# Kernel tuning notes

Measured on AMD Instinct MI355X. Metric: run time of the kernel, lower is better.

Reference implementation:

```python
import jax, jax.numpy as jnp
import numpy as np

N_EMBD = 1024
N_HEAD = 16
HEAD_DIM = N_EMBD // N_HEAD
B, T = 2, 2048
EPS = 1e-5


def setup_inputs() -> dict:
    key = jax.random.key(0)
    ks = jax.random.split(key, 12)
    s = lambda fan_in: 1.0 / np.sqrt(fan_in)
    return {
        "x": jax.random.normal(ks[0], (B, T, N_EMBD), dtype=jnp.float32),
        "ln1_g": jnp.ones((N_EMBD,), jnp.float32),
        "ln1_b": jnp.zeros((N_EMBD,), jnp.float32),
        "W_attn": jax.random.normal(ks[1], (N_EMBD, 3 * N_EMBD), jnp.float32) * s(N_EMBD),
        "b_attn": jnp.zeros((3 * N_EMBD,), jnp.float32),
        "W_proj": jax.random.normal(ks[2], (N_EMBD, N_EMBD), jnp.float32) * s(N_EMBD),
        "b_proj": jnp.zeros((N_EMBD,), jnp.float32),
        "ln2_g": jnp.ones((N_EMBD,), jnp.float32),
        "ln2_b": jnp.zeros((N_EMBD,), jnp.float32),
        "W_fc": jax.random.normal(ks[3], (N_EMBD, 4 * N_EMBD), jnp.float32) * s(N_EMBD),
        "b_fc": jnp.zeros((4 * N_EMBD,), jnp.float32),
        "W_fc2": jax.random.normal(ks[4], (4 * N_EMBD, N_EMBD), jnp.float32) * s(4 * N_EMBD),
        "b_fc2": jnp.zeros((N_EMBD,), jnp.float32),
    }


def _layernorm(x, g, b):
    mu = jnp.mean(x, axis=-1, keepdims=True)
    var = jnp.mean(jnp.square(x - mu), axis=-1, keepdims=True)
    return (x - mu) * jax.lax.rsqrt(var + EPS) * g + b


def _attention(x, W_attn, b_attn, W_proj, b_proj):
    Bsz, Tlen, C = x.shape
    qkv = x @ W_attn + b_attn  # [B,T,3C]
    q, k, v = jnp.split(qkv, 3, axis=-1)
    # [B,H,T,D]
    q = q.reshape(Bsz, Tlen, N_HEAD, HEAD_DIM).transpose(0, 2, 1, 3)
    k = k.reshape(Bsz, Tlen, N_HEAD, HEAD_DIM).transpose(0, 2, 1, 3)
    v = v.reshape(Bsz, Tlen, N_HEAD, HEAD_DIM).transpose(0, 2, 1, 3)
    att = jnp.einsum("bhqd,bhkd->bhqk", q, k) * (HEAD_DIM ** -0.5)
    causal = jnp.tril(jnp.ones((Tlen, Tlen), dtype=bool))
    att = jnp.where(causal[None, None], att, -jnp.inf)
    att = jax.nn.softmax(att, axis=-1)
    y = jnp.einsum("bhqk,bhkd->bhqd", att, v)
    y = y.transpose(0, 2, 1, 3).reshape(Bsz, Tlen, C)
    return y @ W_proj + b_proj


def _mlp(x, W_fc, b_fc, W_fc2, b_fc2):
    h = jax.nn.gelu(x @ W_fc + b_fc, approximate=False)
    return h @ W_fc2 + b_fc2


def reference(x, ln1_g, ln1_b, W_attn, b_attn, W_proj, b_proj,
              ln2_g, ln2_b, W_fc, b_fc, W_fc2, b_fc2):
    x = x + _attention(_layernorm(x, ln1_g, ln1_b), W_attn, b_attn, W_proj, b_proj)
    x = x + _mlp(_layernorm(x, ln2_g, ln2_b), W_fc, b_fc, W_fc2, b_fc2)
    return x
```

## Files before the change

kernel.cpp:

```cpp
#include <hip/hip_runtime.h>
#include <math.h>

typedef unsigned short ushort_t;
typedef __attribute__((ext_vector_type(8))) short f16x8;
typedef __attribute__((ext_vector_type(4))) float f32x4;

#define N_EMBD 1024
#define N_HEAD 16
#define HEAD_DIM 64
#define SEQ_B 2
#define SEQ_T 2048
#define M_TOK (SEQ_B * SEQ_T)

__device__ __forceinline__ ushort_t f2b(float f) {
    union { float f; unsigned int u; } v; v.f = f;
    unsigned int r = (v.u + 0x7FFFu + ((v.u >> 16) & 1u)) >> 16;
    return (ushort_t)r;
}

__device__ __forceinline__ float gelu_fast(float v) {
    float u = v + 0.044715f * v * v * v;
    float e = __expf(-1.5957691216057308f * u);
    return v * __frcp_rn(1.0f + e);
}

__device__ __forceinline__ void gload_lds16(const ushort_t* g, ushort_t* l) {
    __builtin_amdgcn_global_load_lds(
        (const __attribute__((address_space(1))) void*)g,
        (__attribute__((address_space(3))) void*)l, 16, 0, 0);
}

__global__ __launch_bounds__(256) void prep_w(
    const float* __restrict__ Wa, const float* __restrict__ Wp,
    const float* __restrict__ Wf, const float* __restrict__ Wf2,
    ushort_t* __restrict__ Ta, ushort_t* __restrict__ Tp,
    ushort_t* __restrict__ Tf, ushort_t* __restrict__ Tf2,
    const float* __restrict__ x, const float* __restrict__ g1,
    const float* __restrict__ b1, ushort_t* __restrict__ xn) {
    int b = blockIdx.x;
    int t = threadIdx.x;
    if (b >= 12288) {
        int row = b - 12288;
        const float4 v = ((const float4*)(x + (size_t)row * N_EMBD))[t];
        float s = v.x + v.y + v.z + v.w;
        float s2 = v.x * v.x + v.y * v.y + v.z * v.z + v.w * v.w;
        for (int m = 1; m < 64; m <<= 1) {
            s += __shfl_xor(s, m, 64);
            s2 += __shfl_xor(s2, m, 64);
        }
        __shared__ float ss[4], ss2[4];
        if ((t & 63) == 0) { ss[t >> 6] = s; ss2[t >> 6] = s2; }
        __syncthreads();
        s = ss[0] + ss[1] + ss[2] + ss[3];
        s2 = ss2[0] + ss2[1] + ss2[2] + ss2[3];
        float mu = s * (1.0f / N_EMBD);
        float var = s2 * (1.0f / N_EMBD) - mu * mu;
        float rs = rsqrtf(var + 1e-5f);
        const float4 gg = ((const float4*)g1)[t];
        const float4 bb = ((const float4*)b1)[t];
        ushort_t o4[4];
        o4[0] = f2b((v.x - mu) * rs * gg.x + bb.x);
        o4[1] = f2b((v.y - mu) * rs * gg.y + bb.y);
        o4[2] = f2b((v.z - mu) * rs * gg.z + bb.z);
        o4[3] = f2b((v.w - mu) * rs * gg.w + bb.w);
        *(ushort4*)(xn + (size_t)row * N_EMBD + t * 4) = *(ushort4*)o4;
        return;
    }
    __shared__ float tile[32][33];
    const float* W; ushort_t* T; int K, N, nx;
    if (b < 3072)      { W = Wa;  T = Ta;  K = 1024; N = 3072; nx = 96; }
    else if (b < 4096) { W = Wp;  T = Tp;  K = 1024; N = 1024; nx = 32; b -= 3072; }
    else if (b < 8192) { W = Wf;  T = Tf;  K = 1024; N = 4096; nx = 128; b -= 4096; }
    else               { W = Wf2; T = Tf2; K = 4096; N = 1024; nx = 32; b -= 8192; }
    int n0 = (b % nx) * 32, k0 = (b / nx) * 32;
    for (int i = 0; i < 4; ++i) {
        int l = t + i * 256; int r = l >> 5, c2 = l & 31;
        tile[r][c2] = W[(size_t)(k0 + r) * N + n0 + c2];
    }
    __syncthreads();
    for (int i = 0; i < 4; ++i) {
        int l = t + i * 256; int r = l >> 5, c2 = l & 31;
        T[(size_t)(n0 + r) * K + k0 + c2] = f2b(tile[c2][r]);
    }
}

__global__ __launch_bounds__(256) void ln2_kernel(
    const float* __restrict__ x, const float* __restrict__ g,
    const float* __restrict__ b, ushort_t* __restrict__ out) {
    int row = blockIdx.x;
    int t = threadIdx.x;
    const float4 v = ((const float4*)(x + (size_t)row * N_EMBD))[t];
    float s = v.x + v.y + v.z + v.w;
    float s2 = v.x * v.x + v.y * v.y + v.z * v.z + v.w * v.w;
    for (int m = 1; m < 64; m <<= 1) {
        s += __shfl_xor(s, m, 64);
        s2 += __shfl_xor(s2, m, 64);
    }
    __shared__ float ss[4], ss2[4];
    if ((t & 63) == 0) { ss[t >> 6] = s; ss2[t >> 6] = s2; }
    __syncthreads();
    s = ss[0] + ss[1] + ss[2] + ss[3];
    s2 = ss2[0] + ss2[1] + ss2[2] + ss2[3];
    float mu = s * (1.0f / N_EMBD);
    float var = s2 * (1.0f / N_EMBD) - mu * mu;
    float rs = rsqrtf(var + 1e-5f);
    const float4 gg = ((const float4*)g)[t];
    const float4 bb = ((const float4*)b)[t];
    ushort_t o4[4];
    o4[0] = f2b((v.x - mu) * rs * gg.x + bb.x);
    o4[1] = f2b((v.y - mu) * rs * gg.y + bb.y);
    o4[2] = f2b((v.z - mu) * rs * gg.z + bb.z);
    o4[3] = f2b((v.w - mu) * rs * gg.w + bb.w);
    *(ushort4*)(out + (size_t)row * N_EMBD + t * 4) = *(ushort4*)o4;
}

template <int MODE, int NJ>
__device__ __forceinline__ void gemm_epilogue(
    f32x4 (&acc)[4][NJ], const float* __restrict__ bias,
    const float* __restrict__ resid, void* __restrict__ Cout,
    int m0, int n0, int wr, int wc, int quad, int l16, int N) {
    for (int i = 0; i < 4; ++i) {
        for (int j = 0; j < NJ; ++j) {
            int col = n0 + wc + j * 16 + l16;
            float bv = bias[col];
            for (int r = 0; r < 4; ++r) {
                int row = m0 + wr + i * 16 + quad * 4 + r;
                float v = acc[i][j][r] + bv;
                if (MODE == 2) v = gelu_fast(v);
                if (MODE == 1 || MODE == 3) v += resid[(size_t)row * N + col];
                if (MODE == 0 || MODE == 2)
                    ((ushort_t*)Cout)[(size_t)row * N + col] = f2b(v);
                else
                    ((float*)Cout)[(size_t)row * N + col] = v;
            }
        }
    }
}

template <int MODE>
__global__ __launch_bounds__(512) void gemm256(
    const ushort_t* __restrict__ A, const ushort_t* __restrict__ Bt,
    const float* __restrict__ bias, ushort_t* __restrict__ C,
    int M, int N, int K) {
    __shared__ ushort_t As[2][2][8192];
    __shared__ ushort_t Bs[2][2][8192];
    const int t = threadIdx.x, w = t >> 6, lane = t & 63;
    const int quad = lane >> 4, l16 = lane & 15, sw = l16 & 7;
    const int wm = w >> 2, wn = w & 3;
    const int m0 = blockIdx.y * 256, n0 = blockIdx.x * 256;
    const int r8 = lane >> 3, g8 = (lane & 7) ^ r8;
    const ushort_t* Aln = A + (size_t)(m0 + w * 8 + r8) * K + g8 * 8;
    const ushort_t* Bln = Bt + (size_t)(n0 + w * 8 + r8) * K + g8 * 8;

    auto stA = [&](int tk, int h, int buf) {
        const ushort_t* g = Aln + (size_t)(h * 128) * K + tk * 64;
        ushort_t* l = &As[buf][h][w * 512];
        gload_lds16(g, l);
        gload_lds16(g + (size_t)64 * K, l + 4096);
    };
    auto stB = [&](int tk, int h, int buf) {
        const ushort_t* g = Bln + (size_t)(h * 128) * K + tk * 64;
        ushort_t* l = &Bs[buf][h][w * 512];
        gload_lds16(g, l);
        gload_lds16(g + (size_t)64 * K, l + 4096);
    };

    f32x4 acc[8][4] = {};
    f16x8 afr[8][2];

    auto readA = [&](int buf) {
#pragma unroll
        for (int mi = 0; mi < 8; ++mi) {
            afr[mi][0] = *(const f16x8*)&As[buf][wm][(mi * 16 + l16) * 64 + ((quad ^ sw) << 3)];
            afr[mi][1] = *(const f16x8*)&As[buf][wm][(mi * 16 + l16) * 64 + (((4 | quad) ^ sw) << 3)];
        }
    };
    auto rdB = [&](int buf, int nj, int ks) -> f16x8 {
        return *(const f16x8*)&Bs[buf][wn >> 1][((wn & 1) * 64 + nj * 16 + l16) * 64 +
                                               ((((ks << 2) | quad) ^ sw) << 3)];
    };
    auto phase = [&](int buf, int nj, int stK, int stH, int stBuf, int stW, int gate) {
        if (nj == 0) readA(buf);
        f16x8 b0 = rdB(buf, nj, 0), b1 = rdB(buf, nj, 1);
        if (stW == 1) stA(stK, stH, stBuf);
        else if (stW == 2) stB(stK, stH, stBuf);
        asm volatile("s_barrier" ::: "memory");
        __builtin_amdgcn_s_setprio(1);
#pragma unroll
        for (int mi = 0; mi < 8; ++mi) {
            acc[mi][nj] = __builtin_amdgcn_mfma_f32_16x16x32_bf16(afr[mi][0], b0, acc[mi][nj], 0, 0, 0);
            acc[mi][nj] = __builtin_amdgcn_mfma_f32_16x16x32_bf16(afr[mi][1], b1, acc[mi][nj], 0, 0, 0);
        }
        __builtin_amdgcn_s_setprio(0);
        if (gate == 1)
            asm volatile("s_waitcnt vmcnt(4) lgkmcnt(0)\n\ts_barrier" ::: "memory");
        else if (gate == 2)
            asm volatile("s_waitcnt vmcnt(0) lgkmcnt(0)\n\ts_barrier" ::: "memory");
        else
            asm volatile("s_waitcnt lgkmcnt(0)\n\ts_barrier" ::: "memory");
    };

    stA(0, 0, 0); stA(0, 1, 0);
    stB(0, 0, 0); stB(0, 1, 0);
    stA(1, 0, 1); stA(1, 1, 1);
    asm volatile("s_waitcnt vmcnt(4) lgkmcnt(0)\n\ts_barrier" ::: "memory");

    for (int i = 0; i < 7; ++i) {
        const int T0 = 2 * i;
        phase(0, 0, T0 + 1, 0, 1, 2, 0);
        phase(0, 1, T0 + 1, 1, 1, 2, 0);
        phase(0, 2, T0 + 2, 0, 0, 1, 0);
        phase(0, 3, T0 + 2, 1, 0, 1, 1);
        phase(1, 0, T0 + 2, 0, 0, 2, 0);
        phase(1, 1, T0 + 2, 1, 0, 2, 0);
        phase(1, 2, T0 + 3, 0, 1, 1, 0);
        phase(1, 3, T0 + 3, 1, 1, 1, 1);
    }
    phase(0, 0, 15, 0, 1, 2, 0);
    phase(0, 1, 15, 1, 1, 2, 0);
    phase(0, 2, 0, 0, 0, 0, 0);
    phase(0, 3, 0, 0, 0, 0, 2);
    phase(1, 0, 0, 0, 0, 0, 0);
    phase(1, 1, 0, 0, 0, 0, 0);
    phase(1, 2, 0, 0, 0, 0, 0);
    phase(1, 3, 0, 0, 0, 0, 0);

#pragma unroll
    for (int mi = 0; mi < 8; ++mi)
#pragma unroll
        for (int nj = 0; nj < 4; ++nj) {
            int col = n0 + wn * 64 + nj * 16 + l16;
            float bv = bias[col];
#pragma unroll
            for (int r = 0; r < 4; ++r) {
                int row = m0 + wm * 128 + mi * 16 + quad * 4 + r;
                float v = acc[mi][nj][r] + bv;
                if (MODE == 2) v = gelu_fast(v);
                C[(size_t)row * N + col] = f2b(v);
            }
        }
}

template <int MODE>
__device__ __forceinline__ void gemm_body_splitk(
    const ushort_t* __restrict__ A, const ushort_t* __restrict__ Bt,
    const float* __restrict__ bias, const float* __restrict__ resid,
    void* __restrict__ Cout, int M, int N, int K) {
    __shared__ ushort_t As[2][2][128 * 32];
    __shared__ ushort_t Bs[2][2][64 * 32];
    int t = threadIdx.x;
    int wave = t >> 6, lane = t & 63;
    int half = wave >> 2, w4 = wave & 3;
    int quad = lane >> 4, l16 = lane & 15;
    const int swl = (l16 ^ (l16 >> 2)) & 3;
    int wr = (w4 >> 1) * 64, wc = (w4 & 1) * 32;
    const int m0 = blockIdx.y * 128, n0 = blockIdx.x * 64;

    const int K2 = K >> 1;
    const int c = w4 * 64 + lane;
    const int srow = c >> 2, s_l = c & 3;
    const int s_g = s_l ^ ((srow ^ (srow >> 2)) & 3);
    const ushort_t* Ap = &A[(size_t)(m0 + srow) * K + (size_t)half * K2 + s_g * 8];
    const ushort_t* Bp = &Bt[(size_t)(n0 + srow) * K + (size_t)half * K2 + s_g * 8];

    const int NK = K2 >> 5;
    gload_lds16(Ap, &As[0][half][w4 * 512]);
    gload_lds16(Ap + (size_t)64 * K, &As[0][half][w4 * 512 + 2048]);
    gload_lds16(Bp, &Bs[0][half][w4 * 512]);

    f32x4 acc[4][2] = {};
    for (int kt = 0; kt < NK; ++kt) {
        const int cur = kt & 1;
        __syncthreads();
        if (kt + 1 < NK) {
            const int nxt = cur ^ 1;
            const int k0 = (kt + 1) << 5;
            gload_lds16(Ap + k0, &As[nxt][half][w4 * 512]);
            gload_lds16(Ap + (size_t)64 * K + k0, &As[nxt][half][w4 * 512 + 2048]);
            gload_lds16(Bp + k0, &Bs[nxt][half][w4 * 512]);
        }
        f16x8 af[4], bf[2];
        for (int i = 0; i < 4; ++i)
            af[i] = *(const f16x8*)&As[cur][half][(wr + i * 16 + l16) * 32 + (quad ^ swl) * 8];
        for (int j = 0; j < 2; ++j)
            bf[j] = *(const f16x8*)&Bs[cur][half][(wc + j * 16 + l16) * 32 + (quad ^ swl) * 8];
        for (int i = 0; i < 4; ++i)
            for (int j = 0; j < 2; ++j)
                acc[i][j] = __builtin_amdgcn_mfma_f32_16x16x32_bf16(
                    af[i], bf[j], acc[i][j], 0, 0, 0);
    }
    __syncthreads();
    float* red = (float*)&As[0][0][0];
    if (half == 1) {
        for (int i = 0; i < 4; ++i)
            for (int j = 0; j < 2; ++j)
                for (int r = 0; r < 4; ++r)
                    red[(wr + i * 16 + quad * 4 + r) * 64 + wc + j * 16 + l16] =
                        acc[i][j][r];
    }
    __syncthreads();
    if (half == 0) {
        for (int i = 0; i < 4; ++i)
            for (int j = 0; j < 2; ++j)
                for (int r = 0; r < 4; ++r)
                    acc[i][j][r] +=
                        red[(wr + i * 16 + quad * 4 + r) * 64 + wc + j * 16 + l16];
        gemm_epilogue<MODE, 2>(acc, bias, resid, Cout, m0, n0, wr, wc, quad, l16, N);
    }
}

__global__ __launch_bounds__(512) void gemm_proj(
    const ushort_t* A, const ushort_t* Bt, const float* bias,
    const float* resid, void* C, int M, int N, int K) {
    gemm_body_splitk<1>(A, Bt, bias, resid, C, M, N, K); }
__global__ __launch_bounds__(512) void gemm_out(
    const ushort_t* A, const ushort_t* Bt, const float* bias,
    const float* resid, void* C, int M, int N, int K) {
    gemm_body_splitk<3>(A, Bt, bias, resid, C, M, N, K); }

__global__ __launch_bounds__(256) void attn_kernel(
    const ushort_t* __restrict__ qkv, ushort_t* __restrict__ y) {
    const int bh = blockIdx.y;
    const int b = bh >> 4, h = bh & 15;
    const int tok0 = b * SEQ_T;
    const int t = threadIdx.x, wave = t >> 6, lane = t & 63;
    const int quad = lane >> 4, l16 = lane & 15;
    const int sw8 = l16 & 7;
    const size_t ld = 3 * N_EMBD;
    const ushort_t* Qb = qkv + (size_t)tok0 * ld + h * HEAD_DIM;
    const ushort_t* Kb = Qb + N_EMBD;
    const ushort_t* Vb = Qb + 2 * N_EMBD;

    __shared__ ushort_t Ks[2][128 * 64];
    __shared__ ushort_t Vt[64 * 136];
    __shared__ ushort_t Pl[4][16 * 128];

    const int kc = wave * 64 + lane;
    const int kv_s = kc >> 3, ks_l = kc & 7;
    const int ks_g = ks_l ^ (kv_s & 7);
    const ushort_t* KpL = Kb + (size_t)kv_s * ld + ks_g * 8;

    const int v_dcI = t & 7, v_dc = v_dcI * 8;
    int v_kv[4], v_pos[4];
    for (int i = 0; i < 4; ++i) {
        int l = t + i * 256;
        v_kv[i] = l >> 3;
        v_pos[i] = v_kv[i] ^ (v_dcI << 3);
    }

    f16x8 onesB;
    for (int i = 0; i < 8; ++i) onesB[i] = (short)0x3F80;

    for (int phase = 0; phase < 2; ++phase) {
        const int qt = phase == 0 ? (int)blockIdx.x : 31 - (int)blockIdx.x;
        const int q0 = qt * 64;
        const int nkt = (q0 + 191) >> 7;

        const int qrow = q0 + wave * 16 + l16;
        f16x8 qf0 = *(const f16x8*)&Qb[(size_t)qrow * ld + quad * 8];
        f16x8 qf1 = *(const f16x8*)&Qb[(size_t)qrow * ld + 32 + quad * 8];

        f32x4 o[4] = {};
        f32x4 lsum = {};

        __syncthreads();
        gload_lds16(KpL, &Ks[0][wave * 512]);
        gload_lds16(KpL + (size_t)32 * ld, &Ks[0][wave * 512 + 2048]);
        gload_lds16(KpL + (size_t)64 * ld, &Ks[0][wave * 512 + 4096]);
        gload_lds16(KpL + (size_t)96 * ld, &Ks[0][wave * 512 + 6144]);
        for (int i = 0; i < 4; ++i) {
            uint4 r = *(const uint4*)&Vb[(size_t)v_kv[i] * ld + v_dc];
            const ushort_t* pv = (const ushort_t*)&r;
            for (int e = 0; e < 8; ++e)
                Vt[(v_dc + e) * 136 + v_pos[i]] = pv[e];
        }

        for (int kt = 0; kt < nkt; ++kt) {
            const int cur = kt & 1;
            __syncthreads();
            const bool pf = (kt + 1 < nkt);
            uint4 vr[4];
            if (pf) {
                for (int i = 0; i < 4; ++i)
                    vr[i] = *(const uint4*)&Vb[(size_t)((kt + 1) * 128 + v_kv[i]) * ld + v_dc];
                const ushort_t* kp = KpL + (size_t)(kt + 1) * 128 * ld;
                gload_lds16(kp, &Ks[cur ^ 1][wave * 512]);
                gload_lds16(kp + (size_t)32 * ld, &Ks[cur ^ 1][wave * 512 + 2048]);
                gload_lds16(kp + (size_t)64 * ld, &Ks[cur ^ 1][wave * 512 + 4096]);
                gload_lds16(kp + (size_t)96 * ld, &Ks[cur ^ 1][wave * 512 + 6144]);
            }
            f32x4 s[8];
            const int ksl = (quad ^ sw8) << 3;
            __builtin_amdgcn_s_setprio(1);
            for (int j = 0; j < 8; ++j) {
                const int kr = j * 16 + l16;
                f16x8 kf0 = *(const f16x8*)&Ks[cur][kr * 64 + ksl];
                f16x8 kf1 = *(const f16x8*)&Ks[cur][kr * 64 + (ksl ^ 32)];
                f32x4 z = {};
                z = __builtin_amdgcn_mfma_f32_16x16x32_bf16(qf0, kf0, z, 0, 0, 0);
                z = __builtin_amdgcn_mfma_f32_16x16x32_bf16(qf1, kf1, z, 0, 0, 0);
                s[j] = z;
            }
            __builtin_amdgcn_s_setprio(0);
            if (kt == nkt - 1) {
                const int qg = q0 + wave * 16 + quad * 4;
                for (int j = 0; j < 8; ++j) {
                    int kg = kt * 128 + j * 16 + l16;
                    for (int r = 0; r < 4; ++r)
                        if (kg > qg + r) s[j][r] = -INFINITY;
                }
            }
            ushort_t* myP = Pl[wave];
            for (int j = 0; j < 8; ++j) {
                int kvv = j * 16 + l16;
                int chunk = kvv >> 3, klo = kvv & 7;
                for (int r = 0; r < 4; ++r) {
                    float p = __expf(__builtin_fmaf(s[j][r], 0.125f, -20.0f));
                    int q = quad * 4 + r;
                    myP[q * 128 + ((chunk ^ (q & 7)) << 3) + klo] = f2b(p);
                }
            }
            f16x8 pa[4];
            for (int ks = 0; ks < 4; ++ks)
                pa[ks] = *(const f16x8*)&myP[l16 * 128 + ((((ks << 2) | quad) ^ sw8) << 3)];
            __builtin_amdgcn_s_setprio(1);
            for (int ks = 0; ks < 4; ++ks)
                lsum = __builtin_amdgcn_mfma_f32_16x16x32_bf16(pa[ks], onesB, lsum, 0, 0, 0);
            for (int dj = 0; dj < 4; ++dj) {
                const int d = dj * 16 + l16;
                const int dsw3 = (d >> 3) & 7;
                f32x4 oo = o[dj];
                for (int ks = 0; ks < 4; ++ks) {
                    f16x8 vb = *(const f16x8*)&Vt[d * 136 + ((((ks << 2) | quad) ^ dsw3) << 3)];
                    oo = __builtin_amdgcn_mfma_f32_16x16x32_bf16(pa[ks], vb, oo, 0, 0, 0);
                }
                o[dj] = oo;
            }
            __builtin_amdgcn_s_setprio(0);
            if (pf) {
                asm volatile("s_barrier" ::: "memory");
                for (int i = 0; i < 4; ++i) {
                    const ushort_t* pv = (const ushort_t*)&vr[i];
                    for (int e = 0; e < 8; ++e)
                        Vt[(v_dc + e) * 136 + v_pos[i]] = pv[e];
                }
            }
        }
        float rl[4];
        for (int r = 0; r < 4; ++r) rl[r] = __frcp_rn(lsum[r]);
        for (int dj = 0; dj < 4; ++dj)
            for (int r = 0; r < 4; ++r) {
                int row = tok0 + q0 + wave * 16 + quad * 4 + r;
                int col = h * HEAD_DIM + dj * 16 + l16;
                y[(size_t)row * N_EMBD + col] = f2b(o[dj][r] * rl[r]);
            }
    }
}

extern "C" void kernel_launch(void* const* d_in, const int* in_sizes, int n_in,
                              void* d_out, int out_size, void* d_ws, size_t ws_size,
                              hipStream_t stream) {
    const float* x      = (const float*)d_in[0];
    const float* ln1_g  = (const float*)d_in[1];
    const float* ln1_b  = (const float*)d_in[2];
    const float* W_attn = (const float*)d_in[3];
    const float* b_attn = (const float*)d_in[4];
    const float* W_proj = (const float*)d_in[5];
    const float* b_proj = (const float*)d_in[6];
    const float* ln2_g  = (const float*)d_in[7];
    const float* ln2_b  = (const float*)d_in[8];
    const float* W_fc   = (const float*)d_in[9];
    const float* b_fc   = (const float*)d_in[10];
    const float* W_fc2  = (const float*)d_in[11];
    const float* b_fc2  = (const float*)d_in[12];
    float* out = (float*)d_out;

    char* w = (char*)d_ws;
    size_t o = 0;
    ushort_t* xn      = (ushort_t*)(w + o); o += (size_t)M_TOK * N_EMBD * 2;
    ushort_t* qkv     = (ushort_t*)(w + o); o += (size_t)M_TOK * 3 * N_EMBD * 2;
    ushort_t* y       = (ushort_t*)(w + o); o += (size_t)M_TOK * N_EMBD * 2;
    float*    x1      = (float*)(w + o);    o += (size_t)M_TOK * N_EMBD * 4;
    ushort_t* x1n     = (ushort_t*)(w + o); o += (size_t)M_TOK * N_EMBD * 2;
    ushort_t* hbuf    = (ushort_t*)(w + o); o += (size_t)M_TOK * 4 * N_EMBD * 2;
    ushort_t* Wt_attn = (ushort_t*)(w + o); o += (size_t)N_EMBD * 3 * N_EMBD * 2;
    ushort_t* Wt_proj = (ushort_t*)(w + o); o += (size_t)N_EMBD * N_EMBD * 2;
    ushort_t* Wt_fc   = (ushort_t*)(w + o); o += (size_t)N_EMBD * 4 * N_EMBD * 2;
    ushort_t* Wt_fc2  = (ushort_t*)(w + o); o += (size_t)4 * N_EMBD * N_EMBD * 2;

    prep_w<<<12288 + M_TOK, 256, 0, stream>>>(
        W_attn, W_proj, W_fc, W_fc2, Wt_attn, Wt_proj, Wt_fc, Wt_fc2,
        x, ln1_g, ln1_b, xn);
    gemm256<0><<<dim3(3 * N_EMBD / 256, M_TOK / 256), 512, 0, stream>>>(
        xn, Wt_attn, b_attn, qkv, M_TOK, 3 * N_EMBD, N_EMBD);
    attn_kernel<<<dim3(SEQ_T / 128, SEQ_B * N_HEAD), 256, 0, stream>>>(qkv, y);
    gemm_proj<<<dim3(N_EMBD / 64, M_TOK / 128), 512, 0, stream>>>(
        y, Wt_proj, b_proj, x, x1, M_TOK, N_EMBD, N_EMBD);
    ln2_kernel<<<M_TOK, 256, 0, stream>>>(x1, ln2_g, ln2_b, x1n);
    gemm256<2><<<dim3(4 * N_EMBD / 256, M_TOK / 256), 512, 0, stream>>>(
        x1n, Wt_fc, b_fc, hbuf, M_TOK, 4 * N_EMBD, N_EMBD);
    gemm_out<<<dim3(N_EMBD / 64, M_TOK / 128), 512, 0, stream>>>(
        hbuf, Wt_fc2, b_fc2, x1, out, M_TOK, N_EMBD, 4 * N_EMBD);
    (void)in_sizes; (void)n_in; (void)out_size; (void)ws_size;
}
```

Before: 360.0 us.

## Restructure gemm256 main loop to hold B fragments and stream A per phase

Rewrites the 256x256 GEMM inner loop so each K-tile loads all B fragments once and then walks four phases over pairs of A row-blocks, instead of holding all A fragments and streaming B per phase. The prefetch order changes to A-then-B within a tile, and the loop count now comes from K instead of a fixed 7 iterations. This is meant to lower live fragment registers and reshape the LDS-read/MFMA interleave. It also changes the order and wait counts of the global-to-LDS prefetches, which risks a stale or racing buffer if the vmcnt gating does not match the new issue order.

```diff
diff --git a/kernel.cpp b/kernel.cpp
--- a/kernel.cpp
+++ b/kernel.cpp
@@ -137,6 +137,67 @@
     }
 }
 
+template <int GATE, bool DA, bool DB>
+__device__ __forceinline__ void tile4(
+    f32x4 (&acc)[8][4],
+    const ushort_t* __restrict__ Ah,
+    const ushort_t* __restrict__ Bh,
+    int rB, int l16, int quad, int sw, int K,
+    const ushort_t* gA, ushort_t* lA,
+    const ushort_t* gB, ushort_t* lB)
+{
+    const int s0 = (quad ^ sw) << 3, s1 = ((4 | quad) ^ sw) << 3;
+    f16x8 bfr[4][2];
+#pragma unroll
+    for (int j = 0; j < 4; ++j) {
+        const ushort_t* p = &Bh[(rB + j * 16 + l16) * 64];
+        bfr[j][0] = *(const f16x8*)(p + s0);
+        bfr[j][1] = *(const f16x8*)(p + s1);
+    }
+#pragma unroll
+    for (int ph = 0; ph < 4; ++ph) {
+        f16x8 a[2][2];
+#pragma unroll
+        for (int r = 0; r < 2; ++r) {
+            const ushort_t* p = &Ah[((ph * 2 + r) * 16 + l16) * 64];
+            a[r][0] = *(const f16x8*)(p + s0);
+            a[r][1] = *(const f16x8*)(p + s1);
+        }
+        if (DA && ph < 2) {
+            const ushort_t* g = gA + (size_t)(ph * 128) * K;
+            ushort_t* l = lA + ph * 8192;
+            gload_lds16(g, l);
+            gload_lds16(g + (size_t)64 * K, l + 4096);
+        }
+        if (DB && ph >= 2) {
+            const ushort_t* g = gB + (size_t)((ph - 2) * 128) * K;
+            ushort_t* l = lB + (ph - 2) * 8192;
+            gload_lds16(g, l);
+            gload_lds16(g + (size_t)64 * K, l + 4096);
+        }
+        asm volatile("s_barrier" ::: "memory");
+        __builtin_amdgcn_s_setprio(1);
+#pragma unroll
+        for (int r = 0; r < 2; ++r)
+#pragma unroll
+            for (int j = 0; j < 4; ++j) {
+                acc[ph * 2 + r][j] = __builtin_amdgcn_mfma_f32_16x16x32_bf16(
+                    a[r][0], bfr[j][0], acc[ph * 2 + r][j], 0, 0, 0);
+                acc[ph * 2 + r][j] = __builtin_amdgcn_mfma_f32_16x16x32_bf16(
+                    a[r][1], bfr[j][1], acc[ph * 2 + r][j], 0, 0, 0);
+            }
+        __builtin_amdgcn_s_setprio(0);
+        if (ph < 3)
+            asm volatile("s_waitcnt lgkmcnt(0)\n\ts_barrier" ::: "memory");
+        else if (GATE == 1)
+            asm volatile("s_waitcnt vmcnt(4) lgkmcnt(0)\n\ts_barrier" ::: "memory");
+        else if (GATE == 2)
+            asm volatile("s_waitcnt vmcnt(0) lgkmcnt(0)\n\ts_barrier" ::: "memory");
+        else
+            asm volatile("s_waitcnt lgkmcnt(0)\n\ts_barrier" ::: "memory");
+    }
+}
+
 template <int MODE>
 __global__ __launch_bounds__(512) void gemm256(
     const ushort_t* __restrict__ A, const ushort_t* __restrict__ Bt,
@@ -151,79 +212,46 @@
     const int r8 = lane >> 3, g8 = (lane & 7) ^ r8;
     const ushort_t* Aln = A + (size_t)(m0 + w * 8 + r8) * K + g8 * 8;
     const ushort_t* Bln = Bt + (size_t)(n0 + w * 8 + r8) * K + g8 * 8;
-
-    auto stA = [&](int tk, int h, int buf) {
-        const ushort_t* g = Aln + (size_t)(h * 128) * K + tk * 64;
-        ushort_t* l = &As[buf][h][w * 512];
-        gload_lds16(g, l);
-        gload_lds16(g + (size_t)64 * K, l + 4096);
-    };
-    auto stB = [&](int tk, int h, int buf) {
-        const ushort_t* g = Bln + (size_t)(h * 128) * K + tk * 64;
-        ushort_t* l = &Bs[buf][h][w * 512];
-        gload_lds16(g, l);
-        gload_lds16(g + (size_t)64 * K, l + 4096);
-    };
+    ushort_t* sA0 = &As[0][0][w * 512];
+    ushort_t* sA1 = &As[1][0][w * 512];
+    ushort_t* sB0 = &Bs[0][0][w * 512];
+    ushort_t* sB1 = &Bs[1][0][w * 512];
+    const ushort_t* Ah0 = &As[0][wm][0];
+    const ushort_t* Ah1 = &As[1][wm][0];
+    const ushort_t* Bh0 = &Bs[0][wn >> 1][0];
+    const ushort_t* Bh1 = &Bs[1][wn >> 1][0];
+    const int rB = (wn & 1) * 64;
+
+#define STAGE_HALF(gln, tk, h, ldsbase)                                      \
+    do {                                                                     \
+        const ushort_t* _g = (gln) + (size_t)(h) * 128 * K + (tk) * 64;      \
+        ushort_t* _l = (ldsbase) + (h) * 8192;                               \
+        gload_lds16(_g, _l);                                                 \
+        gload_lds16(_g + (size_t)64 * K, _l + 4096);                         \
+    } while (0)
+
+    STAGE_HALF(Aln, 0, 0, sA0); STAGE_HALF(Aln, 0, 1, sA0);
+    STAGE_HALF(Bln, 0, 0, sB0); STAGE_HALF(Bln, 0, 1, sB0);
+    STAGE_HALF(Bln, 1, 0, sB1); STAGE_HALF(Bln, 1, 1, sB1);
+    asm volatile("s_waitcnt vmcnt(4) lgkmcnt(0)\n\ts_barrier" ::: "memory");
+#undef STAGE_HALF
 
     f32x4 acc[8][4] = {};
-    f16x8 afr[8][2];
-
-    auto readA = [&](int buf) {
-#pragma unroll
-        for (int mi = 0; mi < 8; ++mi) {
-            afr[mi][0] = *(const f16x8*)&As[buf][wm][(mi * 16 + l16) * 64 + ((quad ^ sw) << 3)];
-            afr[mi][1] = *(const f16x8*)&As[buf][wm][(mi * 16 + l16) * 64 + (((4 | quad) ^ sw) << 3)];
-        }
-    };
-    auto rdB = [&](int buf, int nj, int ks) -> f16x8 {
-        return *(const f16x8*)&Bs[buf][wn >> 1][((wn & 1) * 64 + nj * 16 + l16) * 64 +
-                                               ((((ks << 2) | quad) ^ sw) << 3)];
-    };
-    auto phase = [&](int buf, int nj, int stK, int stH, int stBuf, int stW, int gate) {
-        if (nj == 0) readA(buf);
-        f16x8 b0 = rdB(buf, nj, 0), b1 = rdB(buf, nj, 1);
-        if (stW == 1) stA(stK, stH, stBuf);
-        else if (stW == 2) stB(stK, stH, stBuf);
-        asm volatile("s_barrier" ::: "memory");
-        __builtin_amdgcn_s_setprio(1);
-#pragma unroll
-        for (int mi = 0; mi < 8; ++mi) {
-            acc[mi][nj] = __builtin_amdgcn_mfma_f32_16x16x32_bf16(afr[mi][0], b0, acc[mi][nj], 0, 0, 0);
-            acc[mi][nj] = __builtin_amdgcn_mfma_f32_16x16x32_bf16(afr[mi][1], b1, acc[mi][nj], 0, 0, 0);
-        }
-        __builtin_amdgcn_s_setprio(0);
-        if (gate == 1)
-            asm volatile("s_waitcnt vmcnt(4) lgkmcnt(0)\n\ts_barrier" ::: "memory");
-        else if (gate == 2)
-            asm volatile("s_waitcnt vmcnt(0) lgkmcnt(0)\n\ts_barrier" ::: "memory");
-        else
-            asm volatile("s_waitcnt lgkmcnt(0)\n\ts_barrier" ::: "memory");
-    };
-
-    stA(0, 0, 0); stA(0, 1, 0);
-    stB(0, 0, 0); stB(0, 1, 0);
-    stA(1, 0, 1); stA(1, 1, 1);
-    asm volatile("s_waitcnt vmcnt(4) lgkmcnt(0)\n\ts_barrier" ::: "memory");
-
-    for (int i = 0; i < 7; ++i) {
-        const int T0 = 2 * i;
-        phase(0, 0, T0 + 1, 0, 1, 2, 0);
-        phase(0, 1, T0 + 1, 1, 1, 2, 0);
-        phase(0, 2, T0 + 2, 0, 0, 1, 0);
-        phase(0, 3, T0 + 2, 1, 0, 1, 1);
-        phase(1, 0, T0 + 2, 0, 0, 2, 0);
-        phase(1, 1, T0 + 2, 1, 0, 2, 0);
-        phase(1, 2, T0 + 3, 0, 1, 1, 0);
-        phase(1, 3, T0 + 3, 1, 1, 1, 1);
-    }
-    phase(0, 0, 15, 0, 1, 2, 0);
-    phase(0, 1, 15, 1, 1, 2, 0);
-    phase(0, 2, 0, 0, 0, 0, 0);
-    phase(0, 3, 0, 0, 0, 0, 2);
-    phase(1, 0, 0, 0, 0, 0, 0);
-    phase(1, 1, 0, 0, 0, 0, 0);
-    phase(1, 2, 0, 0, 0, 0, 0);
-    phase(1, 3, 0, 0, 0, 0, 0);
+    const int NP = (K >> 7) - 1;
+    for (int it = 0; it < NP; ++it) {
+        const int U = 2 * it;
+        tile4<1, true, true>(acc, Ah0, Bh0, rB, l16, quad, sw, K,
+                             Aln + (U + 1) * 64, sA1, Bln + (U + 2) * 64, sB0);
+        tile4<1, true, true>(acc, Ah1, Bh1, rB, l16, quad, sw, K,
+                             Aln + (U + 2) * 64, sA0, Bln + (U + 3) * 64, sB1);
+    }
+    {
+        const int U = 2 * NP;
+        tile4<2, true, false>(acc, Ah0, Bh0, rB, l16, quad, sw, K,
+                              Aln + (U + 1) * 64, sA1, nullptr, nullptr);
+        tile4<0, false, false>(acc, Ah1, Bh1, rB, l16, quad, sw, K,
+                               nullptr, nullptr, nullptr, nullptr);
+    }
 
 #pragma unroll
     for (int mi = 0; mi < 8; ++mi)
```

Result: no change. 353.5 us (-1.8%).
